# Kernel optimization log

Measured on AMD Instinct MI355X. Metric: run time of the kernel, lower is better.

Reference implementation:

```python
import jax, jax.numpy as jnp
import numpy as np


def _normalize_adj(edge_index, num_nodes):
    # add self loops
    loop = jnp.arange(num_nodes, dtype=edge_index.dtype)
    row = jnp.concatenate([edge_index[0], loop])
    col = jnp.concatenate([edge_index[1], loop])
    deg = jax.ops.segment_sum(jnp.ones(row.shape[0], jnp.float32), row,
                              num_segments=num_nodes)
    dis = jnp.where(deg > 0, jax.lax.rsqrt(deg), 0.0)  # deg^{-1/2}, inf->0
    ew = dis[row] * dis[col]
    return row, col, ew


def _gcn_conv(x, W, b, row, col, ew, num_nodes):
    h = x @ W.T + b                       # dense linear [N, out]
    msg = h[col] * ew[:, None]            # gather + scale [E', out]
    return jax.ops.segment_sum(msg, row, num_segments=num_nodes)  # scatter_add


def setup_inputs() -> dict:
    N, E, IN, HID, OUT = 100000, 1600000, 128, 128, 64
    key = jax.random.key(0)
    k1, k2, k3, k4 = jax.random.split(key, 4)
    x = jax.random.normal(k1, (N, IN), jnp.float32)
    edge_index = jax.random.randint(k2, (2, E), 0, N, jnp.int64)
    # xavier_uniform for weights, zero bias (as in reset_parameters)
    lim1 = float(np.sqrt(6.0 / (IN + HID)))
    lim2 = float(np.sqrt(6.0 / (HID + OUT)))
    W1 = jax.random.uniform(k3, (HID, IN), jnp.float32, -lim1, lim1)
    b1 = jnp.zeros((HID,), jnp.float32)
    W2 = jax.random.uniform(k4, (OUT, HID), jnp.float32, -lim2, lim2)
    b2 = jnp.zeros((OUT,), jnp.float32)
    return {"x": x, "edge_index": edge_index, "num_nodes": N,
            "W1": W1, "b1": b1, "W2": W2, "b2": b2}


def reference(x, edge_index, num_nodes, W1, b1, W2, b2):
    row, col, ew = _normalize_adj(edge_index, num_nodes)
    h = _gcn_conv(x, W1, b1, row, col, ew, num_nodes)
    h = jax.nn.relu(h)  # dropout is identity in eval mode
    out = _gcn_conv(h, W2, b2, row, col, ew, num_nodes)
    return out
```

## Files before the change

kernel.cpp:

```cpp
#include <hip/hip_runtime.h>
#include <hip/hip_bf16.h>
#include <stdint.h>


#define TPB 256
#define NBLK_C 256
#define TPB_C 1024
#define MAX_NB 2048

__device__ __forceinline__ float bf16lo(unsigned u) { return __uint_as_float(u << 16); }
__device__ __forceinline__ float bf16hi(unsigned u) { return __uint_as_float(u & 0xffff0000u); }
__device__ __forceinline__ unsigned short f2bf(float f) {
    unsigned u = __float_as_uint(f);
    return (unsigned short)((u + 0x7fff + ((u >> 16) & 1)) >> 16);
}

__global__ void detect64_kernel(const int* __restrict__ ei32, int* __restrict__ flag) {
    if (threadIdx.x == 0 && blockIdx.x == 0) {
        int is64 = 1;
        for (int t = 0; t < 64; ++t) {
            if (ei32[2 * t + 1] != 0) { is64 = 0; break; }
        }
        *flag = is64;
    }
}

__global__ __launch_bounds__(TPB_C) void hist_extract_kernel(const void* __restrict__ ei, int E,
                                                             int CH,
                                                             const int* __restrict__ flag,
                                                             int* __restrict__ row32,
                                                             int* __restrict__ col32,
                                                             int* __restrict__ hist,
                                                             int NB, int N) {
    __shared__ int h[MAX_NB];
    int tid = threadIdx.x;
    for (int bin = tid; bin < NB; bin += TPB_C) h[bin] = 0;
    __syncthreads();

    int b = blockIdx.x;
    int s = b * CH;
    int end = min(E, s + CH);
    int is64 = *flag;
    unsigned uN = (unsigned)N;
    if (is64) {
        const long long* p = (const long long*)ei;
        for (int e = s + tid; e < end; e += TPB_C) {
            int r = (int)p[e];
            int c = (int)p[E + e];
            row32[e] = r;
            col32[e] = c;
            if ((unsigned)r < uN && (unsigned)c < uN) atomicAdd(&h[r >> 7], 1);
        }
    } else {
        const int* p = (const int*)ei;
        for (int e = s + tid; e < end; e += TPB_C) {
            int r = p[e];
            int c = p[E + e];
            row32[e] = r;
            col32[e] = c;
            if ((unsigned)r < uN && (unsigned)c < uN) atomicAdd(&h[r >> 7], 1);
        }
    }
    __syncthreads();
    for (int bin = tid; bin < NB; bin += TPB_C) hist[bin * NBLK_C + b] = h[bin];
}

__global__ __launch_bounds__(NBLK_C) void colscan_kernel(int* __restrict__ hist,
                                                         int* __restrict__ binTotal) {
    __shared__ int sm[NBLK_C];
    int bin = blockIdx.x;
    int tid = threadIdx.x;
    int v = hist[bin * NBLK_C + tid];
    sm[tid] = v;
    __syncthreads();
    for (int o = 1; o < NBLK_C; o <<= 1) {
        int x = (tid >= o) ? sm[tid - o] : 0;
        __syncthreads();
        sm[tid] += x;
        __syncthreads();
    }
    hist[bin * NBLK_C + tid] = sm[tid] - v;
    if (tid == NBLK_C - 1) binTotal[bin] = sm[NBLK_C - 1];
}

__global__ __launch_bounds__(1024) void binscan_kernel(const int* __restrict__ binTotal,
                                                       int* __restrict__ bucketStart, int NB) {
    __shared__ int sm[1024];
    int tid = threadIdx.x;
    int v = (tid < NB) ? binTotal[tid] : 0;
    sm[tid] = v;
    __syncthreads();
    for (int o = 1; o < 1024; o <<= 1) {
        int x = (tid >= o) ? sm[tid - o] : 0;
        __syncthreads();
        sm[tid] += x;
        __syncthreads();
    }
    if (tid < NB) bucketStart[tid] = sm[tid] - v;
}

__global__ __launch_bounds__(TPB_C) void scatter_kernel(const int* __restrict__ row32,
                                                        const int* __restrict__ col32, int E,
                                                        int CH,
                                                        const int* __restrict__ hist,
                                                        const int* __restrict__ bucketStart,
                                                        int* __restrict__ bucketed,
                                                        int NB, int N) {
    __shared__ int cur[MAX_NB];
    int tid = threadIdx.x;
    int b = blockIdx.x;
    for (int bin = tid; bin < NB; bin += TPB_C)
        cur[bin] = bucketStart[bin] + hist[bin * NBLK_C + b];
    __syncthreads();

    int s = b * CH;
    int end = min(E, s + CH);
    unsigned uN = (unsigned)N;
    for (int e = s + tid; e < end; e += TPB_C) {
        int r = row32[e];
        int c = col32[e];
        if ((unsigned)r < uN && (unsigned)c < uN) {
            int pos = atomicAdd(&cur[r >> 7], 1);
            bucketed[pos] = (c << 7) | (r & 127);
        }
    }
}

__global__ __launch_bounds__(TPB) void finecsr_kernel(const int* __restrict__ bucketed,
                                                      const int* __restrict__ bucketStart,
                                                      const int* __restrict__ binTotal,
                                                      int* __restrict__ offs,
                                                      int* __restrict__ cnt,
                                                      float* __restrict__ dis,
                                                      int* __restrict__ csr, int N) {
    __shared__ int c128[128];
    __shared__ int cur128[128];
    __shared__ int sm[TPB];
    int bin = blockIdx.x;
    int tid = threadIdx.x;
    int s = bucketStart[bin];
    int m = binTotal[bin];

    if (tid < 128) c128[tid] = 0;
    __syncthreads();
    for (int i = tid; i < m; i += TPB) atomicAdd(&c128[bucketed[s + i] & 127], 1);
    __syncthreads();

    int v = (tid < 128) ? c128[tid] : 0;
    sm[tid] = v;
    __syncthreads();
    for (int o = 1; o < 128; o <<= 1) {
        int x = (tid >= o) ? sm[tid - o] : 0;
        __syncthreads();
        sm[tid] += x;
        __syncthreads();
    }
    if (tid < 128) {
        int excl = sm[tid] - v;
        int r = bin * 128 + tid;
        if (r < N) {
            offs[r] = s + excl;
            cnt[r] = v;
            dis[r] = rsqrtf((float)v + 1.0f);
        }
        cur128[tid] = s + excl;
    }
    __syncthreads();
    for (int i = tid; i < m; i += TPB) {
        int p = bucketed[s + i];
        int pos = atomicAdd(&cur128[p & 127], 1);
        csr[pos] = p >> 7;
    }
}

template <int BN>
__global__ __launch_bounds__(256, 4) void gemm_tiled_kernel(const float* __restrict__ X,
                                                            const float* __restrict__ W,
                                                            const float* __restrict__ bias,
                                                            const float* __restrict__ dis,
                                                            unsigned short* __restrict__ Hb,
                                                            int N) {
    constexpr int BM = 128, BK = 32, K = 128;
    constexpr int BMp = BM + 4;
    constexpr int BNp = BN + 4;
    constexpr int CN = BN / 16;
    __shared__ float Xs[BK * BMp];
    __shared__ float Ws[BK * BNp];

    const int tid = threadIdx.x;
    const int tx = tid & 15;
    const int ty = tid >> 4;
    const int r0 = blockIdx.x * BM;
    const int lrow = tid >> 3;
    const int kq = tid & 7;

    float acc[8][CN];
#pragma unroll
    for (int r = 0; r < 8; ++r)
#pragma unroll
        for (int c = 0; c < CN; ++c) acc[r][c] = 0.0f;

    const float4* Xv = (const float4*)X;
    const float4* Wv = (const float4*)W;

    for (int k0 = 0; k0 < K; k0 += BK) {
#pragma unroll
        for (int p = 0; p < BM / 32; ++p) {
            int row = lrow + p * 32;
            int rg = r0 + row;
            if (rg >= N) rg = N - 1;
            float4 v = Xv[(size_t)rg * (K / 4) + (k0 >> 2) + kq];
            Xs[(4 * kq + 0) * BMp + row] = v.x;
            Xs[(4 * kq + 1) * BMp + row] = v.y;
            Xs[(4 * kq + 2) * BMp + row] = v.z;
            Xs[(4 * kq + 3) * BMp + row] = v.w;
        }
#pragma unroll
        for (int p = 0; p < BN / 32; ++p) {
            int j = lrow + p * 32;
            float4 v = Wv[(size_t)j * (K / 4) + (k0 >> 2) + kq];
            Ws[(4 * kq + 0) * BNp + j] = v.x;
            Ws[(4 * kq + 1) * BNp + j] = v.y;
            Ws[(4 * kq + 2) * BNp + j] = v.z;
            Ws[(4 * kq + 3) * BNp + j] = v.w;
        }
        __syncthreads();

#pragma unroll 4
        for (int k = 0; k < BK; ++k) {
            float4 xa = *(const float4*)&Xs[k * BMp + 8 * ty];
            float4 xb = *(const float4*)&Xs[k * BMp + 8 * ty + 4];
            float4 wa = *(const float4*)&Ws[k * BNp + 4 * tx];
            float xr[8] = {xa.x, xa.y, xa.z, xa.w, xb.x, xb.y, xb.z, xb.w};
            float wc[CN];
            wc[0] = wa.x; wc[1] = wa.y; wc[2] = wa.z; wc[3] = wa.w;
            if (BN == 128) {
                float4 wb = *(const float4*)&Ws[k * BNp + 64 + 4 * tx];
                wc[4] = wb.x; wc[5] = wb.y; wc[6] = wb.z; wc[7] = wb.w;
            }
#pragma unroll
            for (int r = 0; r < 8; ++r)
#pragma unroll
                for (int c = 0; c < CN; ++c) acc[r][c] += xr[r] * wc[c];
        }
        __syncthreads();
    }

    float4 bva = *(const float4*)&bias[4 * tx];
    float4 bvb = make_float4(0.f, 0.f, 0.f, 0.f);
    if (BN == 128) bvb = *(const float4*)&bias[64 + 4 * tx];
#pragma unroll
    for (int r = 0; r < 8; ++r) {
        int row = r0 + 8 * ty + r;
        if (row < N) {
            float dn = dis[row];
            ushort4 oa;
            oa.x = f2bf((acc[r][0] + bva.x) * dn);
            oa.y = f2bf((acc[r][1] + bva.y) * dn);
            oa.z = f2bf((acc[r][2] + bva.z) * dn);
            oa.w = f2bf((acc[r][3] + bva.w) * dn);
            *(ushort4*)&Hb[(size_t)row * BN + 4 * tx] = oa;
            if (BN == 128) {
                ushort4 ob;
                ob.x = f2bf((acc[r][4] + bvb.x) * dn);
                ob.y = f2bf((acc[r][5] + bvb.y) * dn);
                ob.z = f2bf((acc[r][6] + bvb.z) * dn);
                ob.w = f2bf((acc[r][7] + bvb.w) * dn);
                *(ushort4*)&Hb[(size_t)row * BN + 64 + 4 * tx] = ob;
            }
        }
    }
}

template <int F, bool RELU>
__global__ __launch_bounds__(TPB) void agg_kernel(const unsigned short* __restrict__ Hb,
                                                  const int* __restrict__ csr,
                                                  const int* __restrict__ offs,
                                                  const int* __restrict__ cnt,
                                                  const float* __restrict__ dis,
                                                  float* __restrict__ out, int N) {
    int w = (blockIdx.x * TPB + threadIdx.x) >> 6;
    if (w >= N) return;
    int lane = threadIdx.x & 63;
    float di = dis[w];
    int s = offs[w];
    int d = cnt[w];

    const unsigned* Hu = (const unsigned*)Hb;
    float2 acc;
    if (F == 128) {
        unsigned u = Hu[w * 64 + lane];
        acc.x = bf16lo(u);
        acc.y = bf16hi(u);
    } else {
        acc.x = __uint_as_float(((unsigned)Hb[w * 64 + lane]) << 16);
        acc.y = 0.0f;
    }

    for (int base = 0; base < d; base += 64) {
        int rem = d - base;
        if (rem > 64) rem = 64;
        int cl = (lane < rem) ? csr[s + base + lane] : 0;

        int e = 0;
        for (; e + 8 <= rem; e += 8) {
            int c0 = __shfl(cl, e + 0);
            int c1 = __shfl(cl, e + 1);
            int c2 = __shfl(cl, e + 2);
            int c3 = __shfl(cl, e + 3);
            int c4 = __shfl(cl, e + 4);
            int c5 = __shfl(cl, e + 5);
            int c6 = __shfl(cl, e + 6);
            int c7 = __shfl(cl, e + 7);
            if (F == 128) {
                unsigned u0 = Hu[c0 * 64 + lane];
                unsigned u1 = Hu[c1 * 64 + lane];
                unsigned u2 = Hu[c2 * 64 + lane];
                unsigned u3 = Hu[c3 * 64 + lane];
                unsigned u4 = Hu[c4 * 64 + lane];
                unsigned u5 = Hu[c5 * 64 + lane];
                unsigned u6 = Hu[c6 * 64 + lane];
                unsigned u7 = Hu[c7 * 64 + lane];
                acc.x += ((bf16lo(u0) + bf16lo(u1)) + (bf16lo(u2) + bf16lo(u3))) +
                         ((bf16lo(u4) + bf16lo(u5)) + (bf16lo(u6) + bf16lo(u7)));
                acc.y += ((bf16hi(u0) + bf16hi(u1)) + (bf16hi(u2) + bf16hi(u3))) +
                         ((bf16hi(u4) + bf16hi(u5)) + (bf16hi(u6) + bf16hi(u7)));
            } else {
                float h0 = __uint_as_float(((unsigned)Hb[c0 * 64 + lane]) << 16);
                float h1 = __uint_as_float(((unsigned)Hb[c1 * 64 + lane]) << 16);
                float h2 = __uint_as_float(((unsigned)Hb[c2 * 64 + lane]) << 16);
                float h3 = __uint_as_float(((unsigned)Hb[c3 * 64 + lane]) << 16);
                float h4 = __uint_as_float(((unsigned)Hb[c4 * 64 + lane]) << 16);
                float h5 = __uint_as_float(((unsigned)Hb[c5 * 64 + lane]) << 16);
                float h6 = __uint_as_float(((unsigned)Hb[c6 * 64 + lane]) << 16);
                float h7 = __uint_as_float(((unsigned)Hb[c7 * 64 + lane]) << 16);
                acc.x += ((h0 + h1) + (h2 + h3)) + ((h4 + h5) + (h6 + h7));
            }
        }
        for (; e < rem; ++e) {
            int c0 = __shfl(cl, e);
            if (F == 128) {
                unsigned u0 = Hu[c0 * 64 + lane];
                acc.x += bf16lo(u0);
                acc.y += bf16hi(u0);
            } else {
                acc.x += __uint_as_float(((unsigned)Hb[c0 * 64 + lane]) << 16);
            }
        }
    }

    acc.x *= di;
    acc.y *= di;
    if (RELU) { acc.x = fmaxf(acc.x, 0.f); acc.y = fmaxf(acc.y, 0.f); }
    if (F == 128) {
        ((float2*)out)[w * 64 + lane] = acc;
    } else {
        out[w * 64 + lane] = acc.x;
    }
}

extern "C" void kernel_launch(void* const* d_in, const int* in_sizes, int n_in,
                              void* d_out, int out_size, void* d_ws, size_t ws_size,
                              hipStream_t stream) {
    const float* x  = (const float*)d_in[0];
    const void*  ei = d_in[1];
    const float* W1 = (const float*)d_in[3];
    const float* b1 = (const float*)d_in[4];
    const float* W2 = (const float*)d_in[5];
    const float* b2 = (const float*)d_in[6];
    float* out = (float*)d_out;

    const int IN = 128, HID = 128, OUT = 64;
    const int N = in_sizes[0] / IN;
    const int E = in_sizes[1] / 2;
    const int NB = (N + 127) >> 7;
    const int CH = (E + NBLK_C - 1) / NBLK_C;

    char* ws = (char*)d_ws;
    size_t off = 0;
    auto alloc = [&](size_t bytes) -> void* {
        void* p = (void*)(ws + off);
        off += (bytes + 255) & ~(size_t)255;
        return p;
    };
    int*   flag     = (int*)alloc(256);
    int*   cnt      = (int*)alloc((size_t)N * 4);
    int*   offs     = (int*)alloc((size_t)N * 4);
    float* dis      = (float*)alloc((size_t)N * 4);
    int*   row32    = (int*)alloc((size_t)E * 4);
    int*   col32    = (int*)alloc((size_t)E * 4);
    int*   bucketed = (int*)alloc((size_t)E * 4);
    int*   csr      = (int*)alloc((size_t)E * 4);
    int*   hist     = (int*)alloc((size_t)NB * NBLK_C * 4);
    int*   binTotal = (int*)alloc((size_t)NB * 4);
    int*   bStart   = (int*)alloc((size_t)NB * 4);
    unsigned short* H1b = (unsigned short*)alloc((size_t)N * HID * 2);
    float*          R1  = (float*)alloc((size_t)N * HID * 4);
    unsigned short* H2b = H1b;

    detect64_kernel<<<1, 64, 0, stream>>>((const int*)ei, flag);

    hist_extract_kernel<<<NBLK_C, TPB_C, 0, stream>>>(ei, E, CH, flag, row32, col32,
                                                      hist, NB, N);
    colscan_kernel<<<NB, NBLK_C, 0, stream>>>(hist, binTotal);
    binscan_kernel<<<1, 1024, 0, stream>>>(binTotal, bStart, NB);
    scatter_kernel<<<NBLK_C, TPB_C, 0, stream>>>(row32, col32, E, CH, hist, bStart,
                                                 bucketed, NB, N);
    finecsr_kernel<<<NB, TPB, 0, stream>>>(bucketed, bStart, binTotal,
                                           offs, cnt, dis, csr, N);

    int ngrid = (N + 127) / 128;

    gemm_tiled_kernel<128><<<ngrid, 256, 0, stream>>>(x, W1, b1, dis, H1b, N);
    agg_kernel<128, true><<<(N + 3) / 4, TPB, 0, stream>>>(H1b, csr, offs, cnt, dis, R1, N);

    gemm_tiled_kernel<64><<<ngrid, 256, 0, stream>>>(R1, W2, b2, dis, H2b, N);
    agg_kernel<64, false><<<(N + 3) / 4, TPB, 0, stream>>>(H2b, csr, offs, cnt, dis, out, N);
}
```

Measured before the change: 342.3 us.

## Use bf16 MFMA for dense GEMMs and store layer-1 activations in bf16

Replaces the fp32 shared-memory tiled GEMM with a kernel that converts X and W to bf16 in LDS and computes with 16x16x32 bf16 MFMA instructions, loading the full K=128 at once. The first aggregation now writes its ReLU output as packed bf16 instead of fp32, and the second GEMM reads bf16 input directly. This halves the intermediate activation traffic and moves the matmul onto matrix cores. The cost is reduced precision of the input and intermediate activations and larger LDS use per block. The GEMM output stores are also scalar 16-bit writes, which may coalesce poorly.

```diff
diff --git a/kernel.cpp b/kernel.cpp
--- a/kernel.cpp
+++ b/kernel.cpp
@@ -7,6 +7,9 @@
 #define NBLK_C 256
 #define TPB_C 1024
 #define MAX_NB 2048
+
+typedef __attribute__((ext_vector_type(8))) __bf16 bf16x8;
+typedef __attribute__((ext_vector_type(4))) float f32x4;
 
 __device__ __forceinline__ float bf16lo(unsigned u) { return __uint_as_float(u << 16); }
 __device__ __forceinline__ float bf16hi(unsigned u) { return __uint_as_float(u & 0xffff0000u); }
@@ -173,112 +176,107 @@
     }
 }
 
-template <int BN>
-__global__ __launch_bounds__(256, 4) void gemm_tiled_kernel(const float* __restrict__ X,
-                                                            const float* __restrict__ W,
-                                                            const float* __restrict__ bias,
-                                                            const float* __restrict__ dis,
-                                                            unsigned short* __restrict__ Hb,
-                                                            int N) {
-    constexpr int BM = 128, BK = 32, K = 128;
-    constexpr int BMp = BM + 4;
-    constexpr int BNp = BN + 4;
-    constexpr int CN = BN / 16;
-    __shared__ float Xs[BK * BMp];
-    __shared__ float Ws[BK * BNp];
+template <int BN, bool INB16>
+__global__ __launch_bounds__(256, 2) void gemm_mfma_kernel(const void* __restrict__ Xp,
+                                                           const float* __restrict__ W,
+                                                           const float* __restrict__ bias,
+                                                           const float* __restrict__ dis,
+                                                           unsigned short* __restrict__ Hb,
+                                                           int N) {
+    constexpr int XST = 136;
+    __shared__ unsigned short Xs[128 * XST];
+    __shared__ unsigned short Ws[BN * XST];
 
     const int tid = threadIdx.x;
-    const int tx = tid & 15;
-    const int ty = tid >> 4;
-    const int r0 = blockIdx.x * BM;
-    const int lrow = tid >> 3;
-    const int kq = tid & 7;
-
-    float acc[8][CN];
-#pragma unroll
-    for (int r = 0; r < 8; ++r)
-#pragma unroll
-        for (int c = 0; c < CN; ++c) acc[r][c] = 0.0f;
-
-    const float4* Xv = (const float4*)X;
-    const float4* Wv = (const float4*)W;
-
-    for (int k0 = 0; k0 < K; k0 += BK) {
-#pragma unroll
-        for (int p = 0; p < BM / 32; ++p) {
-            int row = lrow + p * 32;
+    const int r0 = blockIdx.x * 128;
+
+    if (INB16) {
+        const ushort4* Xv = (const ushort4*)Xp;
+        for (int idx = tid; idx < 128 * 32; idx += 256) {
+            int row = idx >> 5, q = idx & 31;
             int rg = r0 + row;
             if (rg >= N) rg = N - 1;
-            float4 v = Xv[(size_t)rg * (K / 4) + (k0 >> 2) + kq];
-            Xs[(4 * kq + 0) * BMp + row] = v.x;
-            Xs[(4 * kq + 1) * BMp + row] = v.y;
-            Xs[(4 * kq + 2) * BMp + row] = v.z;
-            Xs[(4 * kq + 3) * BMp + row] = v.w;
-        }
-#pragma unroll
-        for (int p = 0; p < BN / 32; ++p) {
-            int j = lrow + p * 32;
-            float4 v = Wv[(size_t)j * (K / 4) + (k0 >> 2) + kq];
-            Ws[(4 * kq + 0) * BNp + j] = v.x;
-            Ws[(4 * kq + 1) * BNp + j] = v.y;
-            Ws[(4 * kq + 2) * BNp + j] = v.z;
-            Ws[(4 * kq + 3) * BNp + j] = v.w;
-        }
-        __syncthreads();
-
-#pragma unroll 4
-        for (int k = 0; k < BK; ++k) {
-            float4 xa = *(const float4*)&Xs[k * BMp + 8 * ty];
-            float4 xb = *(const float4*)&Xs[k * BMp + 8 * ty + 4];
-            float4 wa = *(const float4*)&Ws[k * BNp + 4 * tx];
-            float xr[8] = {xa.x, xa.y, xa.z, xa.w, xb.x, xb.y, xb.z, xb.w};
-            float wc[CN];
-            wc[0] = wa.x; wc[1] = wa.y; wc[2] = wa.z; wc[3] = wa.w;
-            if (BN == 128) {
-                float4 wb = *(const float4*)&Ws[k * BNp + 64 + 4 * tx];
-                wc[4] = wb.x; wc[5] = wb.y; wc[6] = wb.z; wc[7] = wb.w;
+            *(ushort4*)&Xs[row * XST + q * 4] = Xv[(size_t)rg * 32 + q];
+        }
+    } else {
+        const float4* Xv = (const float4*)Xp;
+        for (int idx = tid; idx < 128 * 32; idx += 256) {
+            int row = idx >> 5, q = idx & 31;
+            int rg = r0 + row;
+            if (rg >= N) rg = N - 1;
+            float4 v = Xv[(size_t)rg * 32 + q];
+            ushort4 s = make_ushort4(f2bf(v.x), f2bf(v.y), f2bf(v.z), f2bf(v.w));
+            *(ushort4*)&Xs[row * XST + q * 4] = s;
+        }
+    }
+    {
+        const float4* Wv = (const float4*)W;
+        for (int idx = tid; idx < BN * 32; idx += 256) {
+            int n = idx >> 5, q = idx & 31;
+            float4 v = Wv[n * 32 + q];
+            ushort4 s = make_ushort4(f2bf(v.x), f2bf(v.y), f2bf(v.z), f2bf(v.w));
+            *(ushort4*)&Ws[n * XST + q * 4] = s;
+        }
+    }
+    __syncthreads();
+
+    constexpr int RT = (BN == 128) ? 4 : 2;
+    constexpr int CT = 4;
+    const int wave = tid >> 6, lane = tid & 63;
+    const int l15 = lane & 15, q8 = lane >> 4;
+    const int row0 = (BN == 128) ? (wave & 1) * 64 : wave * 32;
+    const int col0 = (BN == 128) ? (wave >> 1) * 64 : 0;
+
+    f32x4 zero = {0.f, 0.f, 0.f, 0.f};
+    f32x4 acc[RT][CT];
+#pragma unroll
+    for (int rt = 0; rt < RT; ++rt)
+#pragma unroll
+        for (int ct = 0; ct < CT; ++ct) acc[rt][ct] = zero;
+
+#pragma unroll
+    for (int ks = 0; ks < 4; ++ks) {
+        int ko = ks * 32 + q8 * 8;
+        bf16x8 a[RT], b[CT];
+#pragma unroll
+        for (int rt = 0; rt < RT; ++rt)
+            a[rt] = *(const bf16x8*)&Xs[(row0 + rt * 16 + l15) * XST + ko];
+#pragma unroll
+        for (int ct = 0; ct < CT; ++ct)
+            b[ct] = *(const bf16x8*)&Ws[(col0 + ct * 16 + l15) * XST + ko];
+#pragma unroll
+        for (int rt = 0; rt < RT; ++rt)
+#pragma unroll
+            for (int ct = 0; ct < CT; ++ct)
+                acc[rt][ct] = __builtin_amdgcn_mfma_f32_16x16x32_bf16(
+                    a[rt], b[ct], acc[rt][ct], 0, 0, 0);
+    }
+
+    float bv[CT];
+#pragma unroll
+    for (int ct = 0; ct < CT; ++ct) bv[ct] = bias[col0 + ct * 16 + l15];
+#pragma unroll
+    for (int rt = 0; rt < RT; ++rt)
+#pragma unroll
+        for (int r = 0; r < 4; ++r) {
+            int row = r0 + row0 + rt * 16 + q8 * 4 + r;
+            if (row < N) {
+                float dn = dis[row];
+#pragma unroll
+                for (int ct = 0; ct < CT; ++ct)
+                    Hb[(size_t)row * BN + col0 + ct * 16 + l15] =
+                        f2bf((acc[rt][ct][r] + bv[ct]) * dn);
             }
-#pragma unroll
-            for (int r = 0; r < 8; ++r)
-#pragma unroll
-                for (int c = 0; c < CN; ++c) acc[r][c] += xr[r] * wc[c];
-        }
-        __syncthreads();
-    }
-
-    float4 bva = *(const float4*)&bias[4 * tx];
-    float4 bvb = make_float4(0.f, 0.f, 0.f, 0.f);
-    if (BN == 128) bvb = *(const float4*)&bias[64 + 4 * tx];
-#pragma unroll
-    for (int r = 0; r < 8; ++r) {
-        int row = r0 + 8 * ty + r;
-        if (row < N) {
-            float dn = dis[row];
-            ushort4 oa;
-            oa.x = f2bf((acc[r][0] + bva.x) * dn);
-            oa.y = f2bf((acc[r][1] + bva.y) * dn);
-            oa.z = f2bf((acc[r][2] + bva.z) * dn);
-            oa.w = f2bf((acc[r][3] + bva.w) * dn);
-            *(ushort4*)&Hb[(size_t)row * BN + 4 * tx] = oa;
-            if (BN == 128) {
-                ushort4 ob;
-                ob.x = f2bf((acc[r][4] + bvb.x) * dn);
-                ob.y = f2bf((acc[r][5] + bvb.y) * dn);
-                ob.z = f2bf((acc[r][6] + bvb.z) * dn);
-                ob.w = f2bf((acc[r][7] + bvb.w) * dn);
-                *(ushort4*)&Hb[(size_t)row * BN + 64 + 4 * tx] = ob;
-            }
-        }
-    }
-}
-
-template <int F, bool RELU>
+        }
+}
+
+template <int F, bool RELU, bool OB16>
 __global__ __launch_bounds__(TPB) void agg_kernel(const unsigned short* __restrict__ Hb,
                                                   const int* __restrict__ csr,
                                                   const int* __restrict__ offs,
                                                   const int* __restrict__ cnt,
                                                   const float* __restrict__ dis,
-                                                  float* __restrict__ out, int N) {
+                                                  void* __restrict__ outp, int N) {
     int w = (blockIdx.x * TPB + threadIdx.x) >> 6;
     if (w >= N) return;
     int lane = threadIdx.x & 63;
@@ -352,10 +350,13 @@
     acc.x *= di;
     acc.y *= di;
     if (RELU) { acc.x = fmaxf(acc.x, 0.f); acc.y = fmaxf(acc.y, 0.f); }
-    if (F == 128) {
-        ((float2*)out)[w * 64 + lane] = acc;
+    if (OB16) {
+        unsigned lo = f2bf(acc.x), hi = f2bf(acc.y);
+        ((unsigned*)outp)[w * 64 + lane] = lo | (hi << 16);
+    } else if (F == 128) {
+        ((float2*)outp)[w * 64 + lane] = acc;
     } else {
-        out[w * 64 + lane] = acc.x;
+        ((float*)outp)[w * 64 + lane] = acc.x;
     }
 }
 
@@ -370,7 +371,7 @@
     const float* b2 = (const float*)d_in[6];
     float* out = (float*)d_out;
 
-    const int IN = 128, HID = 128, OUT = 64;
+    const int IN = 128, HID = 128;
     const int N = in_sizes[0] / IN;
     const int E = in_sizes[1] / 2;
     const int NB = (N + 127) >> 7;
@@ -395,7 +396,7 @@
     int*   binTotal = (int*)alloc((size_t)NB * 4);
     int*   bStart   = (int*)alloc((size_t)NB * 4);
     unsigned short* H1b = (unsigned short*)alloc((size_t)N * HID * 2);
-    float*          R1  = (float*)alloc((size_t)N * HID * 4);
+    unsigned short* R1b = (unsigned short*)alloc((size_t)N * HID * 2);
     unsigned short* H2b = H1b;
 
     detect64_kernel<<<1, 64, 0, stream>>>((const int*)ei, flag);
@@ -411,9 +412,11 @@
 
     int ngrid = (N + 127) / 128;
 
-    gemm_tiled_kernel<128><<<ngrid, 256, 0, stream>>>(x, W1, b1, dis, H1b, N);
-    agg_kernel<128, true><<<(N + 3) / 4, TPB, 0, stream>>>(H1b, csr, offs, cnt, dis, R1, N);
-
-    gemm_tiled_kernel<64><<<ngrid, 256, 0, stream>>>(R1, W2, b2, dis, H2b, N);
-    agg_kernel<64, false><<<(N + 3) / 4, TPB, 0, stream>>>(H2b, csr, offs, cnt, dis, out, N);
-}
+    gemm_mfma_kernel<128, false><<<ngrid, 256, 0, stream>>>(x, W1, b1, dis, H1b, N);
+    agg_kernel<128, true, true><<<(N + 3) / 4, TPB, 0, stream>>>(H1b, csr, offs, cnt,
+                                                                 dis, R1b, N);
+
+    gemm_mfma_kernel<64, true><<<ngrid, 256, 0, stream>>>(R1b, W2, b2, dis, H2b, N);
+    agg_kernel<64, false, false><<<(N + 3) / 4, TPB, 0, stream>>>(H2b, csr, offs, cnt,
+                                                                  dis, out, N);
+}
```

After: 299.7 us. 12.4% less time.
